# Kernel optimization log

Hardware: AMD Instinct MI355X
Metric: run time of the kernel (lower is better)

## Reference

```python
import jax, jax.numpy as jnp
import numpy as np

N_NODES = 100000
N_EDGES = 3200000
IN_CH = 512
HIDDEN = 64
LOC_OUT = 16
OUT_CH = 40


def setup_inputs() -> dict:
    key = jax.random.key(0)
    ks = jax.random.split(key, 10)
    return {
        "batch_x": jax.random.normal(ks[0], (N_NODES, IN_CH), dtype=jnp.float32),
        "edge_index": jax.random.randint(ks[1], (2, N_EDGES), 0, N_NODES, dtype=jnp.int64),
        "glob_emb": jax.random.normal(ks[2], (N_NODES, LOC_OUT), dtype=jnp.float32),
        "W1": jax.random.normal(ks[3], (IN_CH, HIDDEN), dtype=jnp.float32) * (1.0 / np.sqrt(IN_CH)),
        "b1": jnp.zeros((HIDDEN,), dtype=jnp.float32),
        "W2": jax.random.normal(ks[4], (HIDDEN, LOC_OUT), dtype=jnp.float32) * (1.0 / np.sqrt(HIDDEN)),
        "b2": jnp.zeros((LOC_OUT,), dtype=jnp.float32),
        "att_w1": jax.random.normal(ks[5], (LOC_OUT, 16), dtype=jnp.float32) * 0.25,
        "att_b1": jnp.zeros((16,), dtype=jnp.float32),
        "att_w2": jax.random.normal(ks[6], (16, 1), dtype=jnp.float32) * 0.25,
        "lin1_w": jax.random.normal(ks[7], (LOC_OUT, OUT_CH), dtype=jnp.float32) * 0.25,
        "lin1_b": jnp.zeros((OUT_CH,), dtype=jnp.float32),
    }


def _gcn_conv(x, W, b, row, col, n):
    # GCNConv: out = D^-1/2 (A + I) D^-1/2 (X W) + b   (PyG default: self-loops, sym norm)
    h = x @ W
    loops = jnp.arange(n, dtype=row.dtype)
    row2 = jnp.concatenate([row, loops])  # sources (x_j)
    col2 = jnp.concatenate([col, loops])  # targets (aggregation index)
    deg = jax.ops.segment_sum(jnp.ones_like(col2, dtype=h.dtype), col2, num_segments=n)
    dinv = jax.lax.rsqrt(jnp.maximum(deg, 1.0))  # deg >= 1 thanks to self-loops
    norm = dinv[row2] * dinv[col2]               # [E+N]
    agg = jax.ops.segment_sum(h[row2] * norm[:, None], col2, num_segments=n)
    return agg + b


def reference(batch_x, edge_index, glob_emb, W1, b1, W2, b2, att_w1, att_b1, att_w2, lin1_w, lin1_b):
    n = batch_x.shape[0]
    row, col = edge_index[0], edge_index[1]
    x = _gcn_conv(batch_x, W1, b1, row, col, n)
    x = jax.nn.relu(x)  # dropout p=0.0 -> identity
    x = _gcn_conv(x, W2, b2, row, col, n)  # last layer: no relu/dropout
    z = jnp.stack([x, glob_emb], axis=1)  # [N, 2, 16]
    w = jnp.tanh(z @ att_w1 + att_b1) @ att_w2  # [N, 2, 1]
    beta = jax.nn.softmax(w, axis=1)
    emb = jnp.sum(beta * z, axis=1)  # [N, 16]
    return emb @ lin1_w + lin1_b  # [N, 40]
```

## Files before the change

### kernel.cpp

```cpp
#include <hip/hip_runtime.h>

#define N_IN 512
#define HID 64
#define NBLK 256

typedef __attribute__((ext_vector_type(4))) float f32x4;
typedef __attribute__((ext_vector_type(8))) short bf16x8;

__device__ inline float bf2f(unsigned short s) {
    union { unsigned int u; float f; } v; v.u = ((unsigned int)s) << 16; return v.f;
}
__device__ inline unsigned short f2bf(float f) {
    union { float f; unsigned int u; } v; v.f = f;
    unsigned int u = v.u;
    return (unsigned short)((u + 0x7FFFu + ((u >> 16) & 1u)) >> 16);
}

__global__ __launch_bounds__(256) void k_histA_wt(const int* __restrict__ EI, int* __restrict__ hist,
                                                  const float* __restrict__ W1, unsigned short* __restrict__ Wt,
                                                  int E, int N, int K) {
    if (blockIdx.x >= NBLK) {
        int i = (blockIdx.x - NBLK) * 256 + threadIdx.x;
        int k = i >> 6, n = i & 63;
        Wt[n * 512 + k] = f2bf(W1[i]);
        return;
    }
    __shared__ int hs[512];
    __shared__ int sflag;
    if (threadIdx.x == 0) sflag = (EI[1] == 0 && EI[3] == 0 && EI[5] == 0 && EI[7] == 0) ? 1 : 0;
    for (int k = threadIdx.x; k < K; k += 256) hs[k] = 0;
    __syncthreads();
    bool f = sflag != 0;
    int chunk = (E + NBLK - 1) / NBLK;
    int s = blockIdx.x * chunk, e = min(E, s + chunk);
    for (int i = s + threadIdx.x; i < e; i += 256) {
        int c = f ? ((const int2*)EI)[E + i].x : EI[E + i];
        if ((unsigned)c < (unsigned)N) atomicAdd(&hs[c >> 8], 1);
    }
    __syncthreads();
    for (int k = threadIdx.x; k < K; k += 256) hist[k * NBLK + blockIdx.x] = hs[k];
}

__global__ __launch_bounds__(256) void k_scan_a2(const int* __restrict__ in, int* __restrict__ out,
                                                 int* __restrict__ bsum, int n) {
    __shared__ int sd[256];
    int i = blockIdx.x * 256 + threadIdx.x;
    int v = (i < n) ? in[i] : 0;
    sd[threadIdx.x] = v;
    __syncthreads();
    for (int off = 1; off < 256; off <<= 1) {
        int t = 0;
        if (threadIdx.x >= (unsigned)off) t = sd[threadIdx.x - off];
        __syncthreads();
        sd[threadIdx.x] += t;
        __syncthreads();
    }
    if (i < n) out[i] = sd[threadIdx.x] - v;
    if (threadIdx.x == 255) bsum[blockIdx.x] = sd[255];
}

__global__ __launch_bounds__(512) void k_scan_b(const int* __restrict__ bsum, int* __restrict__ bexc, int nb) {
    __shared__ int sd[512];
    int t = threadIdx.x;
    int v = (t < nb) ? bsum[t] : 0;
    sd[t] = v;
    __syncthreads();
    for (int off = 1; off < 512; off <<= 1) {
        int u = 0;
        if (t >= off) u = sd[t - off];
        __syncthreads();
        sd[t] += u;
        __syncthreads();
    }
    if (t < nb) bexc[t] = sd[t] - v;
    if (t == 511) bexc[nb] = sd[511];
}

__global__ __launch_bounds__(256) void k_scan_c2(const int* __restrict__ bexc, int* __restrict__ out,
                                                 int n, int nb) {
    int i = blockIdx.x * 256 + threadIdx.x;
    if (i < n) out[i] += bexc[blockIdx.x];
    if (i == 0) out[n] = bexc[nb];
}

__global__ __launch_bounds__(256) void k_partB_gemm1(const int* __restrict__ EI, const int* __restrict__ histS,
                                                     int* __restrict__ edges2,
                                                     const float* __restrict__ X, const unsigned short* __restrict__ Wt,
                                                     unsigned short* __restrict__ H,
                                                     int E, int N, int K) {
    if (blockIdx.x < NBLK) {
        __shared__ int cur[512];
        __shared__ int sflag;
        if (threadIdx.x == 0) sflag = (EI[1] == 0 && EI[3] == 0 && EI[5] == 0 && EI[7] == 0) ? 1 : 0;
        for (int k = threadIdx.x; k < K; k += 256) cur[k] = histS[k * NBLK + blockIdx.x];
        __syncthreads();
        bool f = sflag != 0;
        int chunk = (E + NBLK - 1) / NBLK;
        int s = blockIdx.x * chunk, e = min(E, s + chunk);
        for (int i = s + threadIdx.x; i < e; i += 256) {
            int r, c;
            if (f) { const int2* E2 = (const int2*)EI; r = E2[i].x; c = E2[E + i].x; }
            else   { r = EI[i]; c = EI[E + i]; }
            if ((unsigned)r >= (unsigned)N || (unsigned)c >= (unsigned)N) continue;
            int pos = atomicAdd(&cur[c >> 8], 1);
            edges2[pos] = r | ((c & 255) << 20);
        }
        return;
    }
    int bb = blockIdx.x - NBLK;
    int tid = threadIdx.x;
    int w = tid >> 6, lane = tid & 63;
    int m_l = lane & 15, q = lane >> 4;
    int m0 = bb * 128 + w * 32;
    int rA0 = m0 + m_l, rA1 = m0 + 16 + m_l;
    int rc0 = rA0 < N ? rA0 : N - 1;
    int rc1 = rA1 < N ? rA1 : N - 1;
    const float* baseA0 = X + (size_t)rc0 * 512 + q * 8;
    const float* baseA1 = X + (size_t)rc1 * 512 + q * 8;
    const unsigned short* baseB = Wt + (size_t)m_l * 512 + q * 8;

    f32x4 acc[2][4] = {};
#pragma unroll 4
    for (int c = 0; c < 16; ++c) {
        int ko = c * 32;
        float4 x0a = *(const float4*)(baseA0 + ko);
        float4 x0b = *(const float4*)(baseA0 + ko + 4);
        float4 x1a = *(const float4*)(baseA1 + ko);
        float4 x1b = *(const float4*)(baseA1 + ko + 4);
        bf16x8 a0, a1;
        a0[0] = (short)f2bf(x0a.x); a0[1] = (short)f2bf(x0a.y); a0[2] = (short)f2bf(x0a.z); a0[3] = (short)f2bf(x0a.w);
        a0[4] = (short)f2bf(x0b.x); a0[5] = (short)f2bf(x0b.y); a0[6] = (short)f2bf(x0b.z); a0[7] = (short)f2bf(x0b.w);
        a1[0] = (short)f2bf(x1a.x); a1[1] = (short)f2bf(x1a.y); a1[2] = (short)f2bf(x1a.z); a1[3] = (short)f2bf(x1a.w);
        a1[4] = (short)f2bf(x1b.x); a1[5] = (short)f2bf(x1b.y); a1[6] = (short)f2bf(x1b.z); a1[7] = (short)f2bf(x1b.w);
#pragma unroll
        for (int t = 0; t < 4; ++t) {
            bf16x8 b = *(const bf16x8*)(baseB + (size_t)t * 16 * 512 + ko);
            acc[0][t] = __builtin_amdgcn_mfma_f32_16x16x32_bf16(a0, b, acc[0][t], 0, 0, 0);
            acc[1][t] = __builtin_amdgcn_mfma_f32_16x16x32_bf16(a1, b, acc[1][t], 0, 0, 0);
        }
    }
#pragma unroll
    for (int h = 0; h < 2; ++h) {
#pragma unroll
        for (int rg = 0; rg < 4; ++rg) {
            int row = m0 + h * 16 + q * 4 + rg;
            if (row < N) {
#pragma unroll
                for (int t = 0; t < 4; ++t)
                    H[(size_t)row * 64 + t * 16 + m_l] = f2bf(acc[h][t][rg]);
            }
        }
    }
}

__global__ __launch_bounds__(256) void k_bucket(const int* __restrict__ histS, const int* __restrict__ edges2,
                                                int* __restrict__ edges, int* __restrict__ start,
                                                float* __restrict__ dinv, unsigned short* __restrict__ H,
                                                int N, int NBtot) {
    __shared__ int hist[256], sd[256], cur[256];
    __shared__ float dvs[256];
    int b = blockIdx.x, tid = threadIdx.x;
    int base = histS[b * NBLK];
    int end  = histS[(b + 1) * NBLK];
    hist[tid] = 0;
    __syncthreads();
    for (int i = base + tid; i < end; i += 256)
        atomicAdd(&hist[(edges2[i] >> 20) & 255], 1);
    __syncthreads();
    int v = hist[tid];
    sd[tid] = v;
    __syncthreads();
    for (int off = 1; off < 256; off <<= 1) {
        int t = 0;
        if (tid >= off) t = sd[tid - off];
        __syncthreads();
        sd[tid] += t;
        __syncthreads();
    }
    int excl = sd[tid] - v;
    cur[tid] = excl;
    int node = b * 256 + tid;
    float dvv = rsqrtf((float)(v + 1));
    dvs[tid] = dvv;
    if (node < N) {
        start[node] = base + excl;
        dinv[node] = dvv;
    }
    if (b == 0 && tid == 0) start[N] = histS[NBtot];
    __syncthreads();
    for (int i = base + tid; i < end; i += 256) {
        int pv = edges2[i];
        int pos = atomicAdd(&cur[(pv >> 20) & 255], 1);
        edges[base + pos] = pv & 0xFFFFF;
    }
    for (int rr = tid >> 4; rr < 256; rr += 16) {
        int n2 = b * 256 + rr;
        if (n2 < N) {
            float dv2 = dvs[rr];
            uint2* pp = (uint2*)(H + (size_t)n2 * 64 + (size_t)(tid & 15) * 4);
            uint2 vv = *pp;
            float f0 = bf2f((unsigned short)(vv.x & 0xffffu)) * dv2;
            float f1 = bf2f((unsigned short)(vv.x >> 16)) * dv2;
            float f2 = bf2f((unsigned short)(vv.y & 0xffffu)) * dv2;
            float f3 = bf2f((unsigned short)(vv.y >> 16)) * dv2;
            vv.x = (unsigned int)f2bf(f0) | ((unsigned int)f2bf(f1) << 16);
            vv.y = (unsigned int)f2bf(f2) | ((unsigned int)f2bf(f3) << 16);
            *pp = vv;
        }
    }
}

__global__ __launch_bounds__(256) void k_agg1g2(const unsigned short* __restrict__ H, const int* __restrict__ edges,
                                                const int* __restrict__ start, const float* __restrict__ dinv,
                                                const float* __restrict__ b1, const float* __restrict__ W2,
                                                unsigned short* __restrict__ H2, int N) {
    __shared__ float w2s[64 * 17];
    int tid = threadIdx.x;
    for (int i = tid; i < 1024; i += 256) { int k = i >> 4, c = i & 15; w2s[k * 17 + c] = W2[i]; }
    __syncthreads();
    int wid = blockIdx.x * 4 + (tid >> 6);
    int lane = tid & 63;
    if (wid >= N) return;
    int g = lane >> 4;
    int c4 = lane & 15;
    const size_t coff = (size_t)c4 * 4;
    float a0 = 0.f, a1 = 0.f, a2 = 0.f, a3 = 0.f;
    int s = start[wid], e = start[wid + 1];
    int i = s;
    if ((i & 3) && i < e) {
        int lim = min(e, (i + 3) & ~3);
        int j = i + g;
        if (j < lim) {
            uint2 v = *(const uint2*)(H + (size_t)edges[j] * 64 + coff);
            a0 += __uint_as_float(v.x << 16);
            a1 += __uint_as_float(v.x & 0xffff0000u);
            a2 += __uint_as_float(v.y << 16);
            a3 += __uint_as_float(v.y & 0xffff0000u);
        }
        i = lim;
    }
    for (; i + 16 <= e; i += 16) {
        int4 sv = *(const int4*)(edges + i + g * 4);
        uint2 v0 = *(const uint2*)(H + (size_t)sv.x * 64 + coff);
        uint2 v1 = *(const uint2*)(H + (size_t)sv.y * 64 + coff);
        uint2 v2 = *(const uint2*)(H + (size_t)sv.z * 64 + coff);
        uint2 v3 = *(const uint2*)(H + (size_t)sv.w * 64 + coff);
        a0 += __uint_as_float(v0.x << 16) + __uint_as_float(v1.x << 16)
            + __uint_as_float(v2.x << 16) + __uint_as_float(v3.x << 16);
        a1 += __uint_as_float(v0.x & 0xffff0000u) + __uint_as_float(v1.x & 0xffff0000u)
            + __uint_as_float(v2.x & 0xffff0000u) + __uint_as_float(v3.x & 0xffff0000u);
        a2 += __uint_as_float(v0.y << 16) + __uint_as_float(v1.y << 16)
            + __uint_as_float(v2.y << 16) + __uint_as_float(v3.y << 16);
        a3 += __uint_as_float(v0.y & 0xffff0000u) + __uint_as_float(v1.y & 0xffff0000u)
            + __uint_as_float(v2.y & 0xffff0000u) + __uint_as_float(v3.y & 0xffff0000u);
    }
    for (; i < e; i += 4) {
        int j = i + g;
        if (j < e) {
            uint2 v = *(const uint2*)(H + (size_t)edges[j] * 64 + coff);
            a0 += __uint_as_float(v.x << 16);
            a1 += __uint_as_float(v.x & 0xffff0000u);
            a2 += __uint_as_float(v.y << 16);
            a3 += __uint_as_float(v.y & 0xffff0000u);
        }
    }
    a0 += __shfl_xor(a0, 16, 64); a0 += __shfl_xor(a0, 32, 64);
    a1 += __shfl_xor(a1, 16, 64); a1 += __shfl_xor(a1, 32, 64);
    a2 += __shfl_xor(a2, 16, 64); a2 += __shfl_xor(a2, 32, 64);
    a3 += __shfl_xor(a3, 16, 64); a3 += __shfl_xor(a3, 32, 64);
    float dv = dinv[wid];
    uint2 sv = *(const uint2*)(H + (size_t)wid * 64 + coff);
    a0 += __uint_as_float(sv.x << 16);
    a1 += __uint_as_float(sv.x & 0xffff0000u);
    a2 += __uint_as_float(sv.y << 16);
    a3 += __uint_as_float(sv.y & 0xffff0000u);
    float4 bv = *(const float4*)(b1 + c4 * 4);
    float r0 = fmaxf(a0 * dv + bv.x, 0.f);
    float r1 = fmaxf(a1 * dv + bv.y, 0.f);
    float r2 = fmaxf(a2 * dv + bv.z, 0.f);
    float r3 = fmaxf(a3 * dv + bv.w, 0.f);
    float p = 0.f;
#pragma unroll
    for (int j = 0; j < 4; ++j) {
        int src = 4 * g + j;
        float x0 = __shfl(r0, src, 64);
        float x1 = __shfl(r1, src, 64);
        float x2 = __shfl(r2, src, 64);
        float x3 = __shfl(r3, src, 64);
        int kb = 16 * g + 4 * j;
        p += x0 * w2s[(kb + 0) * 17 + c4];
        p += x1 * w2s[(kb + 1) * 17 + c4];
        p += x2 * w2s[(kb + 2) * 17 + c4];
        p += x3 * w2s[(kb + 3) * 17 + c4];
    }
    p += __shfl_xor(p, 16, 64);
    p += __shfl_xor(p, 32, 64);
    if (g == 0) H2[(size_t)wid * 16 + c4] = f2bf(p * dv);
}

__global__ __launch_bounds__(256) void k_agg2(const unsigned short* __restrict__ H2, const int* __restrict__ edges,
                                              const int* __restrict__ start, const float* __restrict__ dinv,
                                              const float* __restrict__ b2, float* __restrict__ X2, int N) {
    int wid = blockIdx.x * 4 + (threadIdx.x >> 6);
    int lane = threadIdx.x & 63;
    if (wid >= N) return;
    int g = lane >> 3;
    int c2 = lane & 7;
    const size_t coff = (size_t)c2 * 2;
    float a0 = 0.f, a1 = 0.f;
    int s = start[wid], e = start[wid + 1];
    int i = s;
    if ((i & 3) && i < e) {
        int lim = min(e, (i + 3) & ~3);
        int j = i + g;
        if (j < lim) {
            unsigned int v = *(const unsigned int*)(H2 + (size_t)edges[j] * 16 + coff);
            a0 += __uint_as_float(v << 16);
            a1 += __uint_as_float(v & 0xffff0000u);
        }
        i = lim;
    }
    for (; i + 32 <= e; i += 32) {
        int4 sv = *(const int4*)(edges + i + g * 4);
        unsigned int v0 = *(const unsigned int*)(H2 + (size_t)sv.x * 16 + coff);
        unsigned int v1 = *(const unsigned int*)(H2 + (size_t)sv.y * 16 + coff);
        unsigned int v2 = *(const unsigned int*)(H2 + (size_t)sv.z * 16 + coff);
        unsigned int v3 = *(const unsigned int*)(H2 + (size_t)sv.w * 16 + coff);
        a0 += __uint_as_float(v0 << 16) + __uint_as_float(v1 << 16)
            + __uint_as_float(v2 << 16) + __uint_as_float(v3 << 16);
        a1 += __uint_as_float(v0 & 0xffff0000u) + __uint_as_float(v1 & 0xffff0000u)
            + __uint_as_float(v2 & 0xffff0000u) + __uint_as_float(v3 & 0xffff0000u);
    }
    for (; i < e; i += 8) {
        int j = i + g;
        if (j < e) {
            unsigned int v = *(const unsigned int*)(H2 + (size_t)edges[j] * 16 + coff);
            a0 += __uint_as_float(v << 16);
            a1 += __uint_as_float(v & 0xffff0000u);
        }
    }
    a0 += __shfl_xor(a0, 8, 64); a0 += __shfl_xor(a0, 16, 64); a0 += __shfl_xor(a0, 32, 64);
    a1 += __shfl_xor(a1, 8, 64); a1 += __shfl_xor(a1, 16, 64); a1 += __shfl_xor(a1, 32, 64);
    if (g == 0) {
        float dv = dinv[wid];
        unsigned int sv = *(const unsigned int*)(H2 + (size_t)wid * 16 + coff);
        a0 += __uint_as_float(sv << 16);
        a1 += __uint_as_float(sv & 0xffff0000u);
        float2 bv = *(const float2*)(b2 + c2 * 2);
        float2 o; o.x = a0 * dv + bv.x; o.y = a1 * dv + bv.y;
        *(float2*)(X2 + (size_t)wid * 16 + coff) = o;
    }
}

__global__ __launch_bounds__(256) void k_head(const float* __restrict__ X2, const float* __restrict__ G,
                                              const float* __restrict__ AW1, const float* __restrict__ AB1,
                                              const float* __restrict__ AW2, const float* __restrict__ LW,
                                              const float* __restrict__ LB, float* __restrict__ OUT, int N) {
    __shared__ float s_aw1[256], s_ab1[16], s_aw2[16], s_lw[640], s_lb[40];
    int tid = threadIdx.x;
    s_aw1[tid] = AW1[tid];
    if (tid < 16) { s_ab1[tid] = AB1[tid]; s_aw2[tid] = AW2[tid]; }
    for (int i = tid; i < 640; i += 256) s_lw[i] = LW[i];
    if (tid < 40) s_lb[tid] = LB[tid];
    __syncthreads();
    int node = blockIdx.x * 256 + tid;
    if (node >= N) return;
    float x[16], g[16];
    const float4* xp = (const float4*)(X2 + (size_t)node * 16);
    const float4* gp = (const float4*)(G + (size_t)node * 16);
#pragma unroll
    for (int q = 0; q < 4; ++q) {
        float4 v = xp[q]; x[q*4] = v.x; x[q*4+1] = v.y; x[q*4+2] = v.z; x[q*4+3] = v.w;
        float4 u = gp[q]; g[q*4] = u.x; g[q*4+1] = u.y; g[q*4+2] = u.z; g[q*4+3] = u.w;
    }
    float wx = 0.f, wg = 0.f;
#pragma unroll
    for (int j = 0; j < 16; ++j) {
        float tx = s_ab1[j], tg = s_ab1[j];
#pragma unroll
        for (int c = 0; c < 16; ++c) { tx += x[c] * s_aw1[c*16 + j]; tg += g[c] * s_aw1[c*16 + j]; }
        wx += tanhf(tx) * s_aw2[j];
        wg += tanhf(tg) * s_aw2[j];
    }
    float m = fmaxf(wx, wg);
    float ex = expf(wx - m), eg = expf(wg - m);
    float inv = 1.f / (ex + eg);
    float bx = ex * inv, bg = eg * inv;
    float emb[16];
#pragma unroll
    for (int c = 0; c < 16; ++c) emb[c] = bx * x[c] + bg * g[c];
    float* op = OUT + (size_t)node * 40;
    for (int o = 0; o < 40; ++o) {
        float a = s_lb[o];
#pragma unroll
        for (int c = 0; c < 16; ++c) a += emb[c] * s_lw[c*40 + o];
        op[o] = a;
    }
}

extern "C" void kernel_launch(void* const* d_in, const int* in_sizes, int n_in,
                              void* d_out, int out_size, void* d_ws, size_t ws_size,
                              hipStream_t stream) {
    const float* X   = (const float*)d_in[0];
    const int*   EI  = (const int*)d_in[1];
    const float* G   = (const float*)d_in[2];
    const float* W1  = (const float*)d_in[3];
    const float* B1  = (const float*)d_in[4];
    const float* W2  = (const float*)d_in[5];
    const float* B2  = (const float*)d_in[6];
    const float* AW1 = (const float*)d_in[7];
    const float* AB1 = (const float*)d_in[8];
    const float* AW2 = (const float*)d_in[9];
    const float* LW  = (const float*)d_in[10];
    const float* LB  = (const float*)d_in[11];
    float* OUT = (float*)d_out;

    const int N = in_sizes[0] / N_IN;
    const int E = in_sizes[1] / 2;
    const int NB = (N + 255) / 256;
    const int K  = NB;
    const int NH = K * NBLK;
    const int SB = (NH + 255) / 256;
    const int WB = (N_IN * HID + 255) / 256;
    const int GB = (N + 127) / 128;

    char* w = (char*)d_ws;
    size_t off = 0;
    auto take = [&](size_t bytes) -> void* {
        void* p = (void*)(w + off);
        off = (off + bytes + 255) & ~(size_t)255;
        return p;
    };
    int*   hist   = (int*)take((size_t)NH * 4);
    int*   histS  = (int*)take((size_t)(NH + 1) * 4);
    int*   bsum   = (int*)take((size_t)SB * 4);
    int*   bexc   = (int*)take((size_t)(SB + 1) * 4);
    int*   startp = (int*)take((size_t)(N + 1) * 4);
    float* dinvp  = (float*)take((size_t)N * 4);
    int*   edges2 = (int*)take((size_t)E * 4);
    int*   edges  = (int*)take((size_t)E * 4);
    unsigned short* wt = (unsigned short*)take((size_t)N_IN * HID * 2);
    unsigned short* h1 = (unsigned short*)take((size_t)N * 64 * 2);
    unsigned short* h2 = (unsigned short*)take((size_t)N * 16 * 2);
    float* x2 = (float*)take((size_t)N * 16 * 4);
    (void)ws_size; (void)n_in; (void)out_size;

    k_histA_wt   <<<NBLK + WB, 256, 0, stream>>>(EI, hist, W1, wt, E, N, K);
    k_scan_a2    <<<SB, 256, 0, stream>>>(hist, histS, bsum, NH);
    k_scan_b     <<<1, 512, 0, stream>>>(bsum, bexc, SB);
    k_scan_c2    <<<SB, 256, 0, stream>>>(bexc, histS, NH, SB);
    k_partB_gemm1<<<NBLK + GB, 256, 0, stream>>>(EI, histS, edges2, X, wt, h1, E, N, K);
    k_bucket     <<<K, 256, 0, stream>>>(histS, edges2, edges, startp, dinvp, h1, N, NH);
    k_agg1g2     <<<(N + 3) / 4, 256, 0, stream>>>(h1, edges, startp, dinvp, B1, W2, h2, N);
    k_agg2       <<<(N + 3) / 4, 256, 0, stream>>>(h2, edges, startp, dinvp, B2, x2, N);
    k_head       <<<NB, 256, 0, stream>>>(x2, G, AW1, AB1, AW2, LW, LB, OUT, N);
}
```

Measured before the change: 582.2 us.

## Stage edge partition through LDS sort, split GEMM kernel, unroll aggregation gathers

```diff
diff --git a/kernel.cpp b/kernel.cpp
--- a/kernel.cpp
+++ b/kernel.cpp
@@ -3,6 +3,7 @@
 #define N_IN 512
 #define HID 64
 #define NBLK 256
+#define TILE 2048
 
 typedef __attribute__((ext_vector_type(4))) float f32x4;
 typedef __attribute__((ext_vector_type(8))) short bf16x8;
@@ -28,7 +29,7 @@
     __shared__ int hs[512];
     __shared__ int sflag;
     if (threadIdx.x == 0) sflag = (EI[1] == 0 && EI[3] == 0 && EI[5] == 0 && EI[7] == 0) ? 1 : 0;
-    for (int k = threadIdx.x; k < K; k += 256) hs[k] = 0;
+    for (int k = threadIdx.x; k < 512; k += 256) hs[k] = 0;
     __syncthreads();
     bool f = sflag != 0;
     int chunk = (E + NBLK - 1) / NBLK;
@@ -41,11 +42,10 @@
     for (int k = threadIdx.x; k < K; k += 256) hist[k * NBLK + blockIdx.x] = hs[k];
 }
 
-__global__ __launch_bounds__(256) void k_scan_a2(const int* __restrict__ in, int* __restrict__ out,
-                                                 int* __restrict__ bsum, int n) {
+__global__ __launch_bounds__(256) void k_scan_a2(int* __restrict__ data, int* __restrict__ bsum, int n) {
     __shared__ int sd[256];
     int i = blockIdx.x * 256 + threadIdx.x;
-    int v = (i < n) ? in[i] : 0;
+    int v = (i < n) ? data[i] : 0;
     sd[threadIdx.x] = v;
     __syncthreads();
     for (int off = 1; off < 256; off <<= 1) {
@@ -55,7 +55,7 @@
         sd[threadIdx.x] += t;
         __syncthreads();
     }
-    if (i < n) out[i] = sd[threadIdx.x] - v;
+    if (i < n) data[i] = sd[threadIdx.x] - v;
     if (threadIdx.x == 255) bsum[blockIdx.x] = sd[255];
 }
 
@@ -76,42 +76,80 @@
     if (t == 511) bexc[nb] = sd[511];
 }
 
-__global__ __launch_bounds__(256) void k_scan_c2(const int* __restrict__ bexc, int* __restrict__ out,
-                                                 int n, int nb) {
-    int i = blockIdx.x * 256 + threadIdx.x;
-    if (i < n) out[i] += bexc[blockIdx.x];
-    if (i == 0) out[n] = bexc[nb];
-}
-
-__global__ __launch_bounds__(256) void k_partB_gemm1(const int* __restrict__ EI, const int* __restrict__ histS,
-                                                     int* __restrict__ edges2,
-                                                     const float* __restrict__ X, const unsigned short* __restrict__ Wt,
-                                                     unsigned short* __restrict__ H,
-                                                     int E, int N, int K) {
-    if (blockIdx.x < NBLK) {
-        __shared__ int cur[512];
-        __shared__ int sflag;
-        if (threadIdx.x == 0) sflag = (EI[1] == 0 && EI[3] == 0 && EI[5] == 0 && EI[7] == 0) ? 1 : 0;
-        for (int k = threadIdx.x; k < K; k += 256) cur[k] = histS[k * NBLK + blockIdx.x];
-        __syncthreads();
-        bool f = sflag != 0;
-        int chunk = (E + NBLK - 1) / NBLK;
-        int s = blockIdx.x * chunk, e = min(E, s + chunk);
-        for (int i = s + threadIdx.x; i < e; i += 256) {
+__global__ __launch_bounds__(256) void k_partB(const int* __restrict__ EI, const int* __restrict__ hist,
+                                               const int* __restrict__ bexc, int* __restrict__ edges2,
+                                               int E, int N, int K) {
+    __shared__ int val[TILE];
+    __shared__ unsigned short bkt[TILE];
+    __shared__ int sorted[TILE];
+    __shared__ unsigned short sbkt[TILE];
+    __shared__ int cnt[512], seg[512], cur[512], gcur[512];
+    __shared__ int wsum[4];
+    __shared__ int sflag;
+    int tid = threadIdx.x, b = blockIdx.x;
+    int lane = tid & 63, wv = tid >> 6;
+    if (tid == 0) sflag = (EI[1] == 0 && EI[3] == 0 && EI[5] == 0 && EI[7] == 0) ? 1 : 0;
+    for (int k = tid; k < 512; k += 256) gcur[k] = (k < K) ? (bexc[k] + hist[k * NBLK + b]) : 0;
+    __syncthreads();
+    bool f = sflag != 0;
+    int chunk = (E + NBLK - 1) / NBLK;
+    int s = b * chunk, e = min(E, s + chunk);
+    for (int ts = s; ts < e; ts += TILE) {
+        int n = min(e - ts, TILE);
+        for (int k = tid; k < 512; k += 256) cnt[k] = 0;
+        __syncthreads();
+        for (int i = tid; i < n; i += 256) {
             int r, c;
-            if (f) { const int2* E2 = (const int2*)EI; r = E2[i].x; c = E2[E + i].x; }
-            else   { r = EI[i]; c = EI[E + i]; }
-            if ((unsigned)r >= (unsigned)N || (unsigned)c >= (unsigned)N) continue;
-            int pos = atomicAdd(&cur[c >> 8], 1);
-            edges2[pos] = r | ((c & 255) << 20);
-        }
-        return;
-    }
-    int bb = blockIdx.x - NBLK;
+            if (f) { const int2* E2 = (const int2*)EI; r = E2[ts + i].x; c = E2[E + ts + i].x; }
+            else   { r = EI[ts + i]; c = EI[E + ts + i]; }
+            if ((unsigned)c < (unsigned)N) {
+                unsigned short kb = (unsigned short)(c >> 8);
+                if ((unsigned)r >= (unsigned)N) r = 0;
+                val[i] = r | ((c & 255) << 20);
+                bkt[i] = kb;
+                atomicAdd(&cnt[kb], 1);
+            } else bkt[i] = 0xFFFFu;
+        }
+        __syncthreads();
+        int v0 = cnt[2 * tid], v1 = cnt[2 * tid + 1];
+        int p = v0 + v1, pi = p;
+        for (int d = 1; d < 64; d <<= 1) {
+            int u = __shfl_up(pi, d, 64);
+            if (lane >= d) pi += u;
+        }
+        if (lane == 63) wsum[wv] = pi;
+        __syncthreads();
+        int woff = 0, tot = 0;
+        for (int q = 0; q < 4; ++q) { int t2 = wsum[q]; if (q < wv) woff += t2; tot += t2; }
+        int pe = woff + pi - p;
+        seg[2 * tid] = pe; seg[2 * tid + 1] = pe + v0;
+        cur[2 * tid] = pe; cur[2 * tid + 1] = pe + v0;
+        __syncthreads();
+        for (int i = tid; i < n; i += 256) {
+            unsigned short kb = bkt[i];
+            if (kb != 0xFFFFu) {
+                int pos = atomicAdd(&cur[kb], 1);
+                sorted[pos] = val[i];
+                sbkt[pos] = kb;
+            }
+        }
+        __syncthreads();
+        for (int j = tid; j < tot; j += 256) {
+            int kb = sbkt[j];
+            edges2[gcur[kb] + (j - seg[kb])] = sorted[j];
+        }
+        __syncthreads();
+        for (int k = tid; k < K; k += 256) gcur[k] += cnt[k];
+        __syncthreads();
+    }
+}
+
+__global__ __launch_bounds__(256) void k_gemm1(const float* __restrict__ X, const unsigned short* __restrict__ Wt,
+                                               unsigned short* __restrict__ H, int N) {
     int tid = threadIdx.x;
     int w = tid >> 6, lane = tid & 63;
     int m_l = lane & 15, q = lane >> 4;
-    int m0 = bb * 128 + w * 32;
+    int m0 = blockIdx.x * 128 + w * 32;
     int rA0 = m0 + m_l, rA1 = m0 + 16 + m_l;
     int rc0 = rA0 < N ? rA0 : N - 1;
     int rc1 = rA1 < N ? rA1 : N - 1;
@@ -134,9 +172,9 @@
         a1[4] = (short)f2bf(x1b.x); a1[5] = (short)f2bf(x1b.y); a1[6] = (short)f2bf(x1b.z); a1[7] = (short)f2bf(x1b.w);
 #pragma unroll
         for (int t = 0; t < 4; ++t) {
-            bf16x8 b = *(const bf16x8*)(baseB + (size_t)t * 16 * 512 + ko);
-            acc[0][t] = __builtin_amdgcn_mfma_f32_16x16x32_bf16(a0, b, acc[0][t], 0, 0, 0);
-            acc[1][t] = __builtin_amdgcn_mfma_f32_16x16x32_bf16(a1, b, acc[1][t], 0, 0, 0);
+            bf16x8 bb = *(const bf16x8*)(baseB + (size_t)t * 16 * 512 + ko);
+            acc[0][t] = __builtin_amdgcn_mfma_f32_16x16x32_bf16(a0, bb, acc[0][t], 0, 0, 0);
+            acc[1][t] = __builtin_amdgcn_mfma_f32_16x16x32_bf16(a1, bb, acc[1][t], 0, 0, 0);
         }
     }
 #pragma unroll
@@ -153,15 +191,15 @@
     }
 }
 
-__global__ __launch_bounds__(256) void k_bucket(const int* __restrict__ histS, const int* __restrict__ edges2,
+__global__ __launch_bounds__(256) void k_bucket(const int* __restrict__ bexc, const int* __restrict__ edges2,
                                                 int* __restrict__ edges, int* __restrict__ start,
                                                 float* __restrict__ dinv, unsigned short* __restrict__ H,
-                                                int N, int NBtot) {
+                                                int N, int K) {
     __shared__ int hist[256], sd[256], cur[256];
     __shared__ float dvs[256];
     int b = blockIdx.x, tid = threadIdx.x;
-    int base = histS[b * NBLK];
-    int end  = histS[(b + 1) * NBLK];
+    int base = bexc[b];
+    int end  = bexc[b + 1];
     hist[tid] = 0;
     __syncthreads();
     for (int i = base + tid; i < end; i += 256)
@@ -186,7 +224,7 @@
         start[node] = base + excl;
         dinv[node] = dvv;
     }
-    if (b == 0 && tid == 0) start[N] = histS[NBtot];
+    if (b == 0 && tid == 0) start[N] = bexc[K];
     __syncthreads();
     for (int i = base + tid; i < end; i += 256) {
         int pv = edges2[i];
@@ -239,7 +277,35 @@
         }
         i = lim;
     }
-    for (; i + 16 <= e; i += 16) {
+    for (; i + 32 <= e; i += 32) {
+        int4 s0 = *(const int4*)(edges + i + g * 4);
+        int4 s1 = *(const int4*)(edges + i + 16 + g * 4);
+        uint2 v0 = *(const uint2*)(H + (size_t)s0.x * 64 + coff);
+        uint2 v1 = *(const uint2*)(H + (size_t)s0.y * 64 + coff);
+        uint2 v2 = *(const uint2*)(H + (size_t)s0.z * 64 + coff);
+        uint2 v3 = *(const uint2*)(H + (size_t)s0.w * 64 + coff);
+        uint2 v4 = *(const uint2*)(H + (size_t)s1.x * 64 + coff);
+        uint2 v5 = *(const uint2*)(H + (size_t)s1.y * 64 + coff);
+        uint2 v6 = *(const uint2*)(H + (size_t)s1.z * 64 + coff);
+        uint2 v7 = *(const uint2*)(H + (size_t)s1.w * 64 + coff);
+        a0 += __uint_as_float(v0.x << 16) + __uint_as_float(v1.x << 16)
+            + __uint_as_float(v2.x << 16) + __uint_as_float(v3.x << 16)
+            + __uint_as_float(v4.x << 16) + __uint_as_float(v5.x << 16)
+            + __uint_as_float(v6.x << 16) + __uint_as_float(v7.x << 16);
+        a1 += __uint_as_float(v0.x & 0xffff0000u) + __uint_as_float(v1.x & 0xffff0000u)
+            + __uint_as_float(v2.x & 0xffff0000u) + __uint_as_float(v3.x & 0xffff0000u)
+            + __uint_as_float(v4.x & 0xffff0000u) + __uint_as_float(v5.x & 0xffff0000u)
+            + __uint_as_float(v6.x & 0xffff0000u) + __uint_as_float(v7.x & 0xffff0000u);
+        a2 += __uint_as_float(v0.y << 16) + __uint_as_float(v1.y << 16)
+            + __uint_as_float(v2.y << 16) + __uint_as_float(v3.y << 16)
+            + __uint_as_float(v4.y << 16) + __uint_as_float(v5.y << 16)
+            + __uint_as_float(v6.y << 16) + __uint_as_float(v7.y << 16);
+        a3 += __uint_as_float(v0.y & 0xffff0000u) + __uint_as_float(v1.y & 0xffff0000u)
+            + __uint_as_float(v2.y & 0xffff0000u) + __uint_as_float(v3.y & 0xffff0000u)
+            + __uint_as_float(v4.y & 0xffff0000u) + __uint_as_float(v5.y & 0xffff0000u)
+            + __uint_as_float(v6.y & 0xffff0000u) + __uint_as_float(v7.y & 0xffff0000u);
+    }
+    if (i + 16 <= e) {
         int4 sv = *(const int4*)(edges + i + g * 4);
         uint2 v0 = *(const uint2*)(H + (size_t)sv.x * 64 + coff);
         uint2 v1 = *(const uint2*)(H + (size_t)sv.y * 64 + coff);
@@ -253,6 +319,7 @@
             + __uint_as_float(v2.y << 16) + __uint_as_float(v3.y << 16);
         a3 += __uint_as_float(v0.y & 0xffff0000u) + __uint_as_float(v1.y & 0xffff0000u)
             + __uint_as_float(v2.y & 0xffff0000u) + __uint_as_float(v3.y & 0xffff0000u);
+        i += 16;
     }
     for (; i < e; i += 4) {
         int j = i + g;
@@ -320,7 +387,27 @@
         }
         i = lim;
     }
-    for (; i + 32 <= e; i += 32) {
+    for (; i + 64 <= e; i += 64) {
+        int4 s0 = *(const int4*)(edges + i + g * 4);
+        int4 s1 = *(const int4*)(edges + i + 32 + g * 4);
+        unsigned int v0 = *(const unsigned int*)(H2 + (size_t)s0.x * 16 + coff);
+        unsigned int v1 = *(const unsigned int*)(H2 + (size_t)s0.y * 16 + coff);
+        unsigned int v2 = *(const unsigned int*)(H2 + (size_t)s0.z * 16 + coff);
+        unsigned int v3 = *(const unsigned int*)(H2 + (size_t)s0.w * 16 + coff);
+        unsigned int v4 = *(const unsigned int*)(H2 + (size_t)s1.x * 16 + coff);
+        unsigned int v5 = *(const unsigned int*)(H2 + (size_t)s1.y * 16 + coff);
+        unsigned int v6 = *(const unsigned int*)(H2 + (size_t)s1.z * 16 + coff);
+        unsigned int v7 = *(const unsigned int*)(H2 + (size_t)s1.w * 16 + coff);
+        a0 += __uint_as_float(v0 << 16) + __uint_as_float(v1 << 16)
+            + __uint_as_float(v2 << 16) + __uint_as_float(v3 << 16)
+            + __uint_as_float(v4 << 16) + __uint_as_float(v5 << 16)
+            + __uint_as_float(v6 << 16) + __uint_as_float(v7 << 16);
+        a1 += __uint_as_float(v0 & 0xffff0000u) + __uint_as_float(v1 & 0xffff0000u)
+            + __uint_as_float(v2 & 0xffff0000u) + __uint_as_float(v3 & 0xffff0000u)
+            + __uint_as_float(v4 & 0xffff0000u) + __uint_as_float(v5 & 0xffff0000u)
+            + __uint_as_float(v6 & 0xffff0000u) + __uint_as_float(v7 & 0xffff0000u);
+    }
+    if (i + 32 <= e) {
         int4 sv = *(const int4*)(edges + i + g * 4);
         unsigned int v0 = *(const unsigned int*)(H2 + (size_t)sv.x * 16 + coff);
         unsigned int v1 = *(const unsigned int*)(H2 + (size_t)sv.y * 16 + coff);
@@ -330,6 +417,7 @@
             + __uint_as_float(v2 << 16) + __uint_as_float(v3 << 16);
         a1 += __uint_as_float(v0 & 0xffff0000u) + __uint_as_float(v1 & 0xffff0000u)
             + __uint_as_float(v2 & 0xffff0000u) + __uint_as_float(v3 & 0xffff0000u);
+        i += 32;
     }
     for (; i < e; i += 8) {
         int j = i + g;
@@ -432,7 +520,6 @@
         return p;
     };
     int*   hist   = (int*)take((size_t)NH * 4);
-    int*   histS  = (int*)take((size_t)(NH + 1) * 4);
     int*   bsum   = (int*)take((size_t)SB * 4);
     int*   bexc   = (int*)take((size_t)(SB + 1) * 4);
     int*   startp = (int*)take((size_t)(N + 1) * 4);
@@ -445,13 +532,13 @@
     float* x2 = (float*)take((size_t)N * 16 * 4);
     (void)ws_size; (void)n_in; (void)out_size;
 
-    k_histA_wt   <<<NBLK + WB, 256, 0, stream>>>(EI, hist, W1, wt, E, N, K);
-    k_scan_a2    <<<SB, 256, 0, stream>>>(hist, histS, bsum, NH);
-    k_scan_b     <<<1, 512, 0, stream>>>(bsum, bexc, SB);
-    k_scan_c2    <<<SB, 256, 0, stream>>>(bexc, histS, NH, SB);
-    k_partB_gemm1<<<NBLK + GB, 256, 0, stream>>>(EI, histS, edges2, X, wt, h1, E, N, K);
-    k_bucket     <<<K, 256, 0, stream>>>(histS, edges2, edges, startp, dinvp, h1, N, NH);
-    k_agg1g2     <<<(N + 3) / 4, 256, 0, stream>>>(h1, edges, startp, dinvp, B1, W2, h2, N);
-    k_agg2       <<<(N + 3) / 4, 256, 0, stream>>>(h2, edges, startp, dinvp, B2, x2, N);
-    k_head       <<<NB, 256, 0, stream>>>(x2, G, AW1, AB1, AW2, LW, LB, OUT, N);
-}
+    k_histA_wt<<<NBLK + WB, 256, 0, stream>>>(EI, hist, W1, wt, E, N, K);
+    k_scan_a2 <<<SB, 256, 0, stream>>>(hist, bsum, NH);
+    k_scan_b  <<<1, 512, 0, stream>>>(bsum, bexc, SB);
+    k_partB   <<<NBLK, 256, 0, stream>>>(EI, hist, bexc, edges2, E, N, K);
+    k_gemm1   <<<GB, 256, 0, stream>>>(X, wt, h1, N);
+    k_bucket  <<<K, 256, 0, stream>>>(bexc, edges2, edges, startp, dinvp, h1, N, K);
+    k_agg1g2  <<<(N + 3) / 4, 256, 0, stream>>>(h1, edges, startp, dinvp, B1, W2, h2, N);
+    k_agg2    <<<(N + 3) / 4, 256, 0, stream>>>(h2, edges, startp, dinvp, B2, x2, N);
+    k_head    <<<NB, 256, 0, stream>>>(x2, G, AW1, AB1, AW2, LW, LB, OUT, N);
+}
```

Measured after the change: 613.1 us. +5.3%, slower.
